# Performance work log

Hardware: AMD Instinct MI355X
Metric: run time of the kernel (lower is better)

The kernel has to match this reference:

```python
import jax, jax.numpy as jnp
from jax import lax
import numpy as np


def _lstm_layer(x, Wih, Whh, bih, bhh):
    # x: [B,T,I]; Wih: [4H,I]; Whh: [4H,H]; gate order i,f,g,o (PyTorch).
    B = x.shape[0]
    H = Whh.shape[1]
    xg = jnp.einsum('bti,gi->btg', x, Wih) + bih + bhh  # [B,T,4H]

    def step(carry, xg_t):
        h, c = carry
        g = xg_t + h @ Whh.T  # [B,4H]
        i, f, gg, o = jnp.split(g, 4, axis=-1)
        i = jax.nn.sigmoid(i)
        f = jax.nn.sigmoid(f)
        gg = jnp.tanh(gg)
        o = jax.nn.sigmoid(o)
        c = f * c + i * gg
        h = o * jnp.tanh(c)
        return (h, c), h

    init = (jnp.zeros((B, H), x.dtype), jnp.zeros((B, H), x.dtype))
    _, hs = lax.scan(step, init, jnp.swapaxes(xg, 0, 1))  # hs: [T,B,H]
    return jnp.swapaxes(hs, 0, 1)  # [B,T,H]


def _uniform(key, shape, k):
    return jax.random.uniform(key, shape, jnp.float32, -k, k)


def setup_inputs() -> dict:
    key = jax.random.key(0)
    ks = jax.random.split(key, 20)
    B, T, D = 64, 512, 2048
    x = jax.random.normal(ks[0], (B, T, D), jnp.float32)
    inp = {'x': x}
    # PyTorch LSTM init: U(-1/sqrt(H), 1/sqrt(H))
    specs = [('1', 2048, 256), ('2', 256, 128), ('3', 128, 64)]
    i = 1
    for tag, I, H in specs:
        k = 1.0 / np.sqrt(H)
        inp['Wih' + tag] = _uniform(ks[i], (4 * H, I), k); i += 1
        inp['Whh' + tag] = _uniform(ks[i], (4 * H, H), k); i += 1
        inp['bih' + tag] = _uniform(ks[i], (4 * H,), k); i += 1
        inp['bhh' + tag] = _uniform(ks[i], (4 * H,), k); i += 1
    kd = 1.0 / np.sqrt(64)
    inp['Wd'] = _uniform(ks[13], (32, 64), kd)
    inp['bd'] = _uniform(ks[14], (32,), kd)
    kw = 1.0 / np.sqrt(2048)
    inp['Ww'] = _uniform(ks[15], (32, 2048), kw)
    inp['bw'] = _uniform(ks[16], (32,), kw)
    ko = 1.0 / np.sqrt(64)
    inp['Wo'] = _uniform(ks[17], (1, 64), ko)
    inp['bo'] = _uniform(ks[18], (1,), ko)
    return inp


def reference(x, Wih1, Whh1, bih1, bhh1, Wih2, Whh2, bih2, bhh2,
              Wih3, Whh3, bih3, bhh3, Wd, bd, Ww, bw, Wo, bo):
    out = _lstm_layer(x, Wih1, Whh1, bih1, bhh1)   # [B,T,256]
    out = _lstm_layer(out, Wih2, Whh2, bih2, bhh2)  # [B,T,128]
    out = _lstm_layer(out, Wih3, Whh3, bih3, bhh3)  # [B,T,64]
    deep = out[:, -1, :]                            # dropout is identity at eval
    deep = jax.nn.relu(deep @ Wd.T + bd)            # [B,32]
    wide = x[:, -1, :]
    wide = jax.nn.relu(wide @ Ww.T + bw)            # [B,32]
    comb = jnp.concatenate([deep, wide], axis=1)    # [B,64]
    return comb @ Wo.T + bo                         # [B,1]
```

## Files before the change

### kernel.cpp

```cpp
#include <hip/hip_runtime.h>

typedef _Float16 f16;
typedef _Float16 f16x2 __attribute__((ext_vector_type(2)));
typedef _Float16 f16x8 __attribute__((ext_vector_type(8)));
typedef float    f32x4 __attribute__((ext_vector_type(4)));

__device__ __forceinline__ f16x2 as_h2(unsigned int u) {
  union { unsigned int u; f16x2 h; } c; c.u = u; return c.h;
}
__device__ __forceinline__ unsigned int pack2(float x, float y) {
  union { f16x2 h; unsigned int u; } c; c.h = f16x2{(f16)x, (f16)y}; return c.u;
}
__device__ __forceinline__ float dot2f(unsigned int w, unsigned int h, float acc) {
#if __has_builtin(__builtin_amdgcn_fdot2)
  return __builtin_amdgcn_fdot2(as_h2(w), as_h2(h), acc, false);
#else
  f16x2 a = as_h2(w), b = as_h2(h);
  return acc + (float)a.x * (float)b.x + (float)a.y * (float)b.y;
#endif
}
__device__ __forceinline__ float sigmoidf_(float x) { return 1.f / (1.f + __expf(-x)); }
__device__ __forceinline__ float tanhf_(float x) { float e = __expf(2.f * x); return 1.f - 2.f / (e + 1.f); }

#define GLDS(gsrc, ldst) __builtin_amdgcn_global_load_lds( \
    (const __attribute__((address_space(1))) void*)(gsrc), \
    (__attribute__((address_space(3))) void*)(ldst), 16, 0, 0)

__global__ void cvt_f32_f16(const float* __restrict__ in, f16* __restrict__ out, long n) {
  long i = ((long)blockIdx.x * blockDim.x + threadIdx.x) * 8;
  long stride = (long)gridDim.x * blockDim.x * 8;
  for (; i < n; i += stride) {
    float4 a = *(const float4*)(in + i);
    float4 b = *(const float4*)(in + i + 4);
    f16x8 h = {(f16)a.x, (f16)a.y, (f16)a.z, (f16)a.w,
               (f16)b.x, (f16)b.y, (f16)b.z, (f16)b.w};
    *(f16x8*)(out + i) = h;
  }
}

template<int K>
__global__ __launch_bounds__(256) void gemm_bias(const f16* __restrict__ A,
                                                 const f16* __restrict__ W,
                                                 const float* __restrict__ bias1,
                                                 const float* __restrict__ bias2,
                                                 float* __restrict__ out, int N) {
  constexpr int BK = 32;
  __shared__ f16 As[2][128 * BK];
  __shared__ f16 Bs[2][128 * BK];
  const int tid = threadIdx.x;
  const int wid = tid >> 6, lane = tid & 63;
  const int m0 = blockIdx.x * 128, n0 = blockIdx.y * 128;
  const int wr = (wid >> 1) * 64, wc = (wid & 1) * 64;
  const int r = lane & 15, kg = lane >> 4;

  f32x4 acc[4][4];
  #pragma unroll
  for (int i = 0; i < 4; ++i)
    #pragma unroll
    for (int j = 0; j < 4; ++j) acc[i][j] = f32x4{0.f, 0.f, 0.f, 0.f};

  auto stage = [&](int buf, int k0) {
    #pragma unroll
    for (int i = 0; i < 2; ++i) {
      int c = tid + 256 * i;
      const f16* asrc = A + (long)(m0 + (c >> 2)) * K + k0 + (c & 3) * 8;
      GLDS(asrc, &As[buf][(64 * wid + 256 * i) * 8]);
      const f16* wsrc = W + (long)(n0 + (c >> 2)) * K + k0 + (c & 3) * 8;
      GLDS(wsrc, &Bs[buf][(64 * wid + 256 * i) * 8]);
    }
  };

  stage(0, 0);
  for (int kt = 0; kt < K / BK; ++kt) {
    __syncthreads();
    if (kt + 1 < K / BK) stage((kt + 1) & 1, (kt + 1) * BK);
    const f16* Ab = As[kt & 1];
    const f16* Bb = Bs[kt & 1];
    f16x8 af[4], bf[4];
    #pragma unroll
    for (int f = 0; f < 4; ++f) {
      af[f] = *(const f16x8*)&Ab[(wr + f * 16 + r) * BK + kg * 8];
      bf[f] = *(const f16x8*)&Bb[(wc + f * 16 + r) * BK + kg * 8];
    }
    #pragma unroll
    for (int mf = 0; mf < 4; ++mf)
      #pragma unroll
      for (int nf = 0; nf < 4; ++nf)
        acc[mf][nf] = __builtin_amdgcn_mfma_f32_16x16x32_f16(af[mf], bf[nf], acc[mf][nf], 0, 0, 0);
  }

  #pragma unroll
  for (int nf = 0; nf < 4; ++nf) {
    int n = n0 + wc + nf * 16 + r;
    float bsum = bias1[n] + bias2[n];
    #pragma unroll
    for (int mf = 0; mf < 4; ++mf) {
      #pragma unroll
      for (int q = 0; q < 4; ++q) {
        int m = m0 + wr + mf * 16 + kg * 4 + q;
        out[(long)m * N + n] = acc[mf][nf][q] + bsum;
      }
    }
  }
}

__global__ __launch_bounds__(512, 2) void lstm_l1(const float* __restrict__ xg,
                                                  const float* __restrict__ Whh,
                                                  f16* __restrict__ hout) {
  __shared__ uint2 wtail[18][1024];
  __shared__ uint4 hbuf[32];
  __shared__ float gact[1024];
  const int b = blockIdx.x;
  const int t = threadIdx.x;
  const int g0 = t, g1 = t + 512;

  unsigned int w0[92], w1[92];
  #pragma unroll
  for (int p = 0; p < 92; ++p) {
    float2 f0 = *(const float2*)&Whh[g0 * 256 + 2 * p];
    float2 f1 = *(const float2*)&Whh[g1 * 256 + 2 * p];
    w0[p] = pack2(f0.x, f0.y);
    w1[p] = pack2(f1.x, f1.y);
  }
  #pragma unroll
  for (int u = 0; u < 18; ++u) {
    float4 f0 = *(const float4*)&Whh[g0 * 256 + 184 + 4 * u];
    wtail[u][g0] = make_uint2(pack2(f0.x, f0.y), pack2(f0.z, f0.w));
    float4 f1 = *(const float4*)&Whh[g1 * 256 + 184 + 4 * u];
    wtail[u][g1] = make_uint2(pack2(f1.x, f1.y), pack2(f1.z, f1.w));
  }
  if (t < 32) hbuf[t] = make_uint4(0, 0, 0, 0);
  float c = 0.f;
  __syncthreads();

  const bool g1_sig = (t >= 256);
  const long rowbase = (long)b * 512;
  float a0 = xg[rowbase * 1024 + g0];
  float a1 = xg[rowbase * 1024 + g1];
  for (int ts = 0; ts < 512; ++ts) {
    const long base = rowbase + ts;
    const long nb = rowbase + (ts < 511 ? ts + 1 : 511);
    float a0n = xg[nb * 1024 + g0];
    float a1n = xg[nb * 1024 + g1];
    float s0 = 0.f, s1 = 0.f;
    #pragma unroll
    for (int i = 0; i < 23; ++i) {
      uint4 hv = hbuf[i];
      if (i & 1) {
        s0 = dot2f(w0[4 * i + 0], hv.x, s0); s0 = dot2f(w0[4 * i + 1], hv.y, s0);
        s0 = dot2f(w0[4 * i + 2], hv.z, s0); s0 = dot2f(w0[4 * i + 3], hv.w, s0);
        s1 = dot2f(w1[4 * i + 0], hv.x, s1); s1 = dot2f(w1[4 * i + 1], hv.y, s1);
        s1 = dot2f(w1[4 * i + 2], hv.z, s1); s1 = dot2f(w1[4 * i + 3], hv.w, s1);
      } else {
        a0 = dot2f(w0[4 * i + 0], hv.x, a0); a0 = dot2f(w0[4 * i + 1], hv.y, a0);
        a0 = dot2f(w0[4 * i + 2], hv.z, a0); a0 = dot2f(w0[4 * i + 3], hv.w, a0);
        a1 = dot2f(w1[4 * i + 0], hv.x, a1); a1 = dot2f(w1[4 * i + 1], hv.y, a1);
        a1 = dot2f(w1[4 * i + 2], hv.z, a1); a1 = dot2f(w1[4 * i + 3], hv.w, a1);
      }
    }
    #pragma unroll
    for (int j = 0; j < 9; ++j) {
      uint4 hv = hbuf[23 + j];
      uint2 wa0 = wtail[2 * j][g0], wb0 = wtail[2 * j + 1][g0];
      uint2 wa1 = wtail[2 * j][g1], wb1 = wtail[2 * j + 1][g1];
      if (j & 1) {
        s0 = dot2f(wa0.x, hv.x, s0); s0 = dot2f(wa0.y, hv.y, s0);
        s0 = dot2f(wb0.x, hv.z, s0); s0 = dot2f(wb0.y, hv.w, s0);
        s1 = dot2f(wa1.x, hv.x, s1); s1 = dot2f(wa1.y, hv.y, s1);
        s1 = dot2f(wb1.x, hv.z, s1); s1 = dot2f(wb1.y, hv.w, s1);
      } else {
        a0 = dot2f(wa0.x, hv.x, a0); a0 = dot2f(wa0.y, hv.y, a0);
        a0 = dot2f(wb0.x, hv.z, a0); a0 = dot2f(wb0.y, hv.w, a0);
        a1 = dot2f(wa1.x, hv.x, a1); a1 = dot2f(wa1.y, hv.y, a1);
        a1 = dot2f(wb1.x, hv.z, a1); a1 = dot2f(wb1.y, hv.w, a1);
      }
    }
    a0 += s0; a1 += s1;
    gact[g0] = sigmoidf_(a0);
    gact[g1] = g1_sig ? sigmoidf_(a1) : tanhf_(a1);
    __syncthreads();
    if (t < 256) {
      float i_ = gact[t], f_ = gact[256 + t], gg = gact[512 + t], o_ = gact[768 + t];
      c = f_ * c + i_ * gg;
      float hn = o_ * tanhf_(c);
      reinterpret_cast<f16*>(hbuf)[t] = (f16)hn;
      hout[base * 256 + t] = (f16)hn;
    }
    __syncthreads();
    a0 = a0n; a1 = a1n;
  }
}

__global__ __launch_bounds__(512) void lstm_l2(const float* __restrict__ xg,
                                               const float* __restrict__ Whh,
                                               f16* __restrict__ hout) {
  __shared__ uint4 hbuf[16];
  __shared__ float gact[512];
  const int b = blockIdx.x, t = threadIdx.x;
  unsigned int w[64];
  #pragma unroll
  for (int p = 0; p < 64; ++p) {
    float2 f = *(const float2*)&Whh[t * 128 + 2 * p];
    w[p] = pack2(f.x, f.y);
  }
  if (t < 16) hbuf[t] = make_uint4(0, 0, 0, 0);
  float c = 0.f;
  __syncthreads();
  const int type = t >> 7;
  const long rowbase = (long)b * 512;
  float a = xg[rowbase * 512 + t];
  for (int ts = 0; ts < 512; ++ts) {
    const long base = rowbase + ts;
    const long nb = rowbase + (ts < 511 ? ts + 1 : 511);
    float an = xg[nb * 512 + t];
    float s = 0.f;
    #pragma unroll
    for (int i = 0; i < 16; ++i) {
      uint4 hv = hbuf[i];
      if (i & 1) {
        s = dot2f(w[4 * i + 0], hv.x, s); s = dot2f(w[4 * i + 1], hv.y, s);
        s = dot2f(w[4 * i + 2], hv.z, s); s = dot2f(w[4 * i + 3], hv.w, s);
      } else {
        a = dot2f(w[4 * i + 0], hv.x, a); a = dot2f(w[4 * i + 1], hv.y, a);
        a = dot2f(w[4 * i + 2], hv.z, a); a = dot2f(w[4 * i + 3], hv.w, a);
      }
    }
    a += s;
    gact[t] = (type == 2) ? tanhf_(a) : sigmoidf_(a);
    __syncthreads();
    if (t < 128) {
      float i_ = gact[t], f_ = gact[128 + t], gg = gact[256 + t], o_ = gact[384 + t];
      c = f_ * c + i_ * gg;
      float hn = o_ * tanhf_(c);
      reinterpret_cast<f16*>(hbuf)[t] = (f16)hn;
      hout[base * 128 + t] = (f16)hn;
    }
    __syncthreads();
    a = an;
  }
}

__global__ __launch_bounds__(256) void lstm_l3(const float* __restrict__ xg,
                                               const float* __restrict__ Whh,
                                               float* __restrict__ h3last) {
  __shared__ uint4 hbuf[8];
  __shared__ float gact[256];
  const int b = blockIdx.x, t = threadIdx.x;
  unsigned int w[32];
  #pragma unroll
  for (int p = 0; p < 32; ++p) {
    float2 f = *(const float2*)&Whh[t * 64 + 2 * p];
    w[p] = pack2(f.x, f.y);
  }
  if (t < 8) hbuf[t] = make_uint4(0, 0, 0, 0);
  float c = 0.f;
  __syncthreads();
  const int type = t >> 6;
  const long rowbase = (long)b * 512;
  float a = xg[rowbase * 256 + t];
  for (int ts = 0; ts < 512; ++ts) {
    const long nb = rowbase + (ts < 511 ? ts + 1 : 511);
    float an = xg[nb * 256 + t];
    float s = 0.f;
    #pragma unroll
    for (int i = 0; i < 8; ++i) {
      uint4 hv = hbuf[i];
      if (i & 1) {
        s = dot2f(w[4 * i + 0], hv.x, s); s = dot2f(w[4 * i + 1], hv.y, s);
        s = dot2f(w[4 * i + 2], hv.z, s); s = dot2f(w[4 * i + 3], hv.w, s);
      } else {
        a = dot2f(w[4 * i + 0], hv.x, a); a = dot2f(w[4 * i + 1], hv.y, a);
        a = dot2f(w[4 * i + 2], hv.z, a); a = dot2f(w[4 * i + 3], hv.w, a);
      }
    }
    a += s;
    gact[t] = (type == 2) ? tanhf_(a) : sigmoidf_(a);
    __syncthreads();
    if (t < 64) {
      float i_ = gact[t], f_ = gact[64 + t], gg = gact[128 + t], o_ = gact[192 + t];
      c = f_ * c + i_ * gg;
      float hn = o_ * tanhf_(c);
      reinterpret_cast<f16*>(hbuf)[t] = (f16)hn;
      if (ts == 511) h3last[b * 64 + t] = hn;
    }
    __syncthreads();
    a = an;
  }
}

__global__ __launch_bounds__(256) void head_kernel(const float* __restrict__ x,
                                                   const float* __restrict__ h3last,
                                                   const float* __restrict__ Wd, const float* __restrict__ bd,
                                                   const float* __restrict__ Ww, const float* __restrict__ bw,
                                                   const float* __restrict__ Wo, const float* __restrict__ bo,
                                                   float* __restrict__ outp) {
  __shared__ float part[256];
  __shared__ float comb[64];
  const int b = blockIdx.x, t = threadIdx.x;
  const int o = t & 31, seg = t >> 5;
  const float* xl = x + ((long)b * 512 + 511) * 2048;
  float s = 0.f;
  for (int k = seg * 256; k < seg * 256 + 256; ++k) s += xl[k] * Ww[o * 2048 + k];
  part[t] = s;
  __syncthreads();
  if (t < 32) {
    float w = 0.f;
    #pragma unroll
    for (int q = 0; q < 8; ++q) w += part[t + 32 * q];
    w += bw[t];
    comb[32 + t] = fmaxf(w, 0.f);
    float d = bd[t];
    for (int k = 0; k < 64; ++k) d += h3last[b * 64 + k] * Wd[t * 64 + k];
    comb[t] = fmaxf(d, 0.f);
  }
  __syncthreads();
  if (t == 0) {
    float r = bo[0];
    for (int j = 0; j < 64; ++j) r += comb[j] * Wo[j];
    outp[b] = r;
  }
}

static inline int cvt_blocks(long n) {
  long bl = (n / 8 + 255) / 256;
  return (int)(bl > 4096 ? 4096 : bl);
}

extern "C" void kernel_launch(void* const* d_in, const int* in_sizes, int n_in,
                              void* d_out, int out_size, void* d_ws, size_t ws_size,
                              hipStream_t stream) {
  const float* x    = (const float*)d_in[0];
  const float* Wih1 = (const float*)d_in[1];
  const float* Whh1 = (const float*)d_in[2];
  const float* bih1 = (const float*)d_in[3];
  const float* bhh1 = (const float*)d_in[4];
  const float* Wih2 = (const float*)d_in[5];
  const float* Whh2 = (const float*)d_in[6];
  const float* bih2 = (const float*)d_in[7];
  const float* bhh2 = (const float*)d_in[8];
  const float* Wih3 = (const float*)d_in[9];
  const float* Whh3 = (const float*)d_in[10];
  const float* bih3 = (const float*)d_in[11];
  const float* bhh3 = (const float*)d_in[12];
  const float* Wd   = (const float*)d_in[13];
  const float* bd   = (const float*)d_in[14];
  const float* Ww   = (const float*)d_in[15];
  const float* bw   = (const float*)d_in[16];
  const float* Wo   = (const float*)d_in[17];
  const float* bo   = (const float*)d_in[18];

  char* ws = (char*)d_ws;
  f16*   x_h   = (f16*)(ws + 0);
  float* xg1   = (float*)(ws + 134217728);
  f16*   h1    = (f16*)(ws + 268435456);
  f16*   wih1h = (f16*)(ws + 285212672);
  f16*   wih2h = (f16*)(ws + 289406976);
  f16*   wih3h = (f16*)(ws + 289669120);
  float* h3l   = (float*)(ws + 289734656);
  float* xg2   = (float*)(ws + 0);
  f16*   h2    = (f16*)(ws + 134217728);
  float* xg3   = (float*)(ws + 67108864);

  cvt_f32_f16<<<cvt_blocks(67108864), 256, 0, stream>>>(x, x_h, 67108864L);
  cvt_f32_f16<<<cvt_blocks(2097152), 256, 0, stream>>>(Wih1, wih1h, 2097152L);
  cvt_f32_f16<<<cvt_blocks(131072), 256, 0, stream>>>(Wih2, wih2h, 131072L);
  cvt_f32_f16<<<cvt_blocks(32768), 256, 0, stream>>>(Wih3, wih3h, 32768L);

  gemm_bias<2048><<<dim3(256, 8), 256, 0, stream>>>(x_h, wih1h, bih1, bhh1, xg1, 1024);
  lstm_l1<<<64, 512, 0, stream>>>(xg1, Whh1, h1);
  gemm_bias<256><<<dim3(256, 4), 256, 0, stream>>>(h1, wih2h, bih2, bhh2, xg2, 512);
  lstm_l2<<<64, 512, 0, stream>>>(xg2, Whh2, h2);
  gemm_bias<128><<<dim3(256, 2), 256, 0, stream>>>(h2, wih3h, bih3, bhh3, xg3, 256);
  lstm_l3<<<64, 256, 0, stream>>>(xg3, Whh3, h3l);
  head_kernel<<<64, 256, 0, stream>>>(x, h3l, Wd, bd, Ww, bw, Wo, bo, (float*)d_out);
}
```

Measured before the change: 2.308 ms.

## Run layer-1 LSTM recurrence with one gate row per thread over 1024 threads

The layer-1 recurrent kernel now launches 1024 threads per block, with each thread owning a single gate row instead of two. Each thread keeps 192 of its 256 weights in registers and reads the remaining 64 from LDS. The hidden-state buffer is double-buffered so the next h is written into the other slot. This roughly halves the serial dot-product chain per thread and doubles parallelism per step. In exchange, register pressure per thread goes up and barriers now synchronise more waves per block.

```diff
diff --git a/kernel.cpp b/kernel.cpp
--- a/kernel.cpp
+++ b/kernel.cpp
@@ -104,90 +104,73 @@
   }
 }
 
-__global__ __launch_bounds__(512, 2) void lstm_l1(const float* __restrict__ xg,
-                                                  const float* __restrict__ Whh,
-                                                  f16* __restrict__ hout) {
-  __shared__ uint2 wtail[18][1024];
-  __shared__ uint4 hbuf[32];
+__global__ __launch_bounds__(1024, 4) void lstm_l1(const float* __restrict__ xg,
+                                                   const float* __restrict__ Whh,
+                                                   f16* __restrict__ hout) {
+  __shared__ uint2 wl2[16][1024];
+  __shared__ uint4 hb[2][32];
   __shared__ float gact[1024];
-  const int b = blockIdx.x;
-  const int t = threadIdx.x;
-  const int g0 = t, g1 = t + 512;
-
-  unsigned int w0[92], w1[92];
-  #pragma unroll
-  for (int p = 0; p < 92; ++p) {
-    float2 f0 = *(const float2*)&Whh[g0 * 256 + 2 * p];
-    float2 f1 = *(const float2*)&Whh[g1 * 256 + 2 * p];
-    w0[p] = pack2(f0.x, f0.y);
-    w1[p] = pack2(f1.x, f1.y);
-  }
-  #pragma unroll
-  for (int u = 0; u < 18; ++u) {
-    float4 f0 = *(const float4*)&Whh[g0 * 256 + 184 + 4 * u];
-    wtail[u][g0] = make_uint2(pack2(f0.x, f0.y), pack2(f0.z, f0.w));
-    float4 f1 = *(const float4*)&Whh[g1 * 256 + 184 + 4 * u];
-    wtail[u][g1] = make_uint2(pack2(f1.x, f1.y), pack2(f1.z, f1.w));
-  }
-  if (t < 32) hbuf[t] = make_uint4(0, 0, 0, 0);
+  const int b = blockIdx.x, t = threadIdx.x;
+
+  unsigned int w[96];
+  #pragma unroll
+  for (int p = 0; p < 48; ++p) {
+    float4 f = *(const float4*)&Whh[t * 256 + 4 * p];
+    w[2 * p]     = pack2(f.x, f.y);
+    w[2 * p + 1] = pack2(f.z, f.w);
+  }
+  #pragma unroll
+  for (int u = 0; u < 16; ++u) {
+    float4 f = *(const float4*)&Whh[t * 256 + 192 + 4 * u];
+    wl2[u][t] = make_uint2(pack2(f.x, f.y), pack2(f.z, f.w));
+  }
+  if (t < 32) hb[0][t] = make_uint4(0, 0, 0, 0);
   float c = 0.f;
   __syncthreads();
 
-  const bool g1_sig = (t >= 256);
+  const int type = t >> 8;
   const long rowbase = (long)b * 512;
-  float a0 = xg[rowbase * 1024 + g0];
-  float a1 = xg[rowbase * 1024 + g1];
+  float a = xg[rowbase * 1024 + t];
   for (int ts = 0; ts < 512; ++ts) {
+    const int p = ts & 1;
     const long base = rowbase + ts;
-    const long nb = rowbase + (ts < 511 ? ts + 1 : 511);
-    float a0n = xg[nb * 1024 + g0];
-    float a1n = xg[nb * 1024 + g1];
-    float s0 = 0.f, s1 = 0.f;
-    #pragma unroll
-    for (int i = 0; i < 23; ++i) {
-      uint4 hv = hbuf[i];
+    float an = xg[(base + (ts < 511 ? 1 : 0)) * 1024 + t];
+    float s = 0.f;
+    #pragma unroll
+    for (int i = 0; i < 24; ++i) {
+      uint4 hv = hb[p][i];
       if (i & 1) {
-        s0 = dot2f(w0[4 * i + 0], hv.x, s0); s0 = dot2f(w0[4 * i + 1], hv.y, s0);
-        s0 = dot2f(w0[4 * i + 2], hv.z, s0); s0 = dot2f(w0[4 * i + 3], hv.w, s0);
-        s1 = dot2f(w1[4 * i + 0], hv.x, s1); s1 = dot2f(w1[4 * i + 1], hv.y, s1);
-        s1 = dot2f(w1[4 * i + 2], hv.z, s1); s1 = dot2f(w1[4 * i + 3], hv.w, s1);
+        s = dot2f(w[4 * i + 0], hv.x, s); s = dot2f(w[4 * i + 1], hv.y, s);
+        s = dot2f(w[4 * i + 2], hv.z, s); s = dot2f(w[4 * i + 3], hv.w, s);
       } else {
-        a0 = dot2f(w0[4 * i + 0], hv.x, a0); a0 = dot2f(w0[4 * i + 1], hv.y, a0);
-        a0 = dot2f(w0[4 * i + 2], hv.z, a0); a0 = dot2f(w0[4 * i + 3], hv.w, a0);
-        a1 = dot2f(w1[4 * i + 0], hv.x, a1); a1 = dot2f(w1[4 * i + 1], hv.y, a1);
-        a1 = dot2f(w1[4 * i + 2], hv.z, a1); a1 = dot2f(w1[4 * i + 3], hv.w, a1);
-      }
-    }
-    #pragma unroll
-    for (int j = 0; j < 9; ++j) {
-      uint4 hv = hbuf[23 + j];
-      uint2 wa0 = wtail[2 * j][g0], wb0 = wtail[2 * j + 1][g0];
-      uint2 wa1 = wtail[2 * j][g1], wb1 = wtail[2 * j + 1][g1];
-      if (j & 1) {
-        s0 = dot2f(wa0.x, hv.x, s0); s0 = dot2f(wa0.y, hv.y, s0);
-        s0 = dot2f(wb0.x, hv.z, s0); s0 = dot2f(wb0.y, hv.w, s0);
-        s1 = dot2f(wa1.x, hv.x, s1); s1 = dot2f(wa1.y, hv.y, s1);
-        s1 = dot2f(wb1.x, hv.z, s1); s1 = dot2f(wb1.y, hv.w, s1);
+        a = dot2f(w[4 * i + 0], hv.x, a); a = dot2f(w[4 * i + 1], hv.y, a);
+        a = dot2f(w[4 * i + 2], hv.z, a); a = dot2f(w[4 * i + 3], hv.w, a);
+      }
+    }
+    #pragma unroll
+    for (int q = 0; q < 8; ++q) {
+      uint4 hv = hb[p][24 + q];
+      uint2 wa = wl2[2 * q][t], wb = wl2[2 * q + 1][t];
+      if (q & 1) {
+        s = dot2f(wa.x, hv.x, s); s = dot2f(wa.y, hv.y, s);
+        s = dot2f(wb.x, hv.z, s); s = dot2f(wb.y, hv.w, s);
       } else {
-        a0 = dot2f(wa0.x, hv.x, a0); a0 = dot2f(wa0.y, hv.y, a0);
-        a0 = dot2f(wb0.x, hv.z, a0); a0 = dot2f(wb0.y, hv.w, a0);
-        a1 = dot2f(wa1.x, hv.x, a1); a1 = dot2f(wa1.y, hv.y, a1);
-        a1 = dot2f(wb1.x, hv.z, a1); a1 = dot2f(wb1.y, hv.w, a1);
-      }
-    }
-    a0 += s0; a1 += s1;
-    gact[g0] = sigmoidf_(a0);
-    gact[g1] = g1_sig ? sigmoidf_(a1) : tanhf_(a1);
+        a = dot2f(wa.x, hv.x, a); a = dot2f(wa.y, hv.y, a);
+        a = dot2f(wb.x, hv.z, a); a = dot2f(wb.y, hv.w, a);
+      }
+    }
+    a += s;
+    gact[t] = (type == 2) ? tanhf_(a) : sigmoidf_(a);
     __syncthreads();
     if (t < 256) {
       float i_ = gact[t], f_ = gact[256 + t], gg = gact[512 + t], o_ = gact[768 + t];
       c = f_ * c + i_ * gg;
       float hn = o_ * tanhf_(c);
-      reinterpret_cast<f16*>(hbuf)[t] = (f16)hn;
+      reinterpret_cast<f16*>(hb[p ^ 1])[t] = (f16)hn;
       hout[base * 256 + t] = (f16)hn;
     }
     __syncthreads();
-    a0 = a0n; a1 = a1n;
+    a = an;
   }
 }
 
@@ -367,7 +350,7 @@
   cvt_f32_f16<<<cvt_blocks(32768), 256, 0, stream>>>(Wih3, wih3h, 32768L);
 
   gemm_bias<2048><<<dim3(256, 8), 256, 0, stream>>>(x_h, wih1h, bih1, bhh1, xg1, 1024);
-  lstm_l1<<<64, 512, 0, stream>>>(xg1, Whh1, h1);
+  lstm_l1<<<64, 1024, 0, stream>>>(xg1, Whh1, h1);
   gemm_bias<256><<<dim3(256, 4), 256, 0, stream>>>(h1, wih2h, bih2, bhh2, xg2, 512);
   lstm_l2<<<64, 512, 0, stream>>>(xg2, Whh2, h2);
   gemm_bias<128><<<dim3(256, 2), 256, 0, stream>>>(h2, wih3h, bih3, bhh3, xg3, 256);
```

New measurement: 2.455 ms. +6.4%, slower.
